# Optimization experiments

Measured on AMD Instinct MI355X. Metric: run time of the kernel, lower is better.

The kernel has to match this reference:

```python
import jax, jax.numpy as jnp
import numpy as np

K = 7        # kernel_size
G = 16       # group_number
STRIDE = 1
BN_EPS = 1e-5


def setup_inputs() -> dict:
    key = jax.random.key(0)
    ks = jax.random.split(key, 3)
    B, C, H, W = 2, 256, 56, 56
    Cr = C // 4  # reduction_ratio = 4
    x = jax.random.normal(ks[0], (B, C, H, W), dtype=jnp.float32)
    w1 = jax.random.normal(ks[1], (Cr, C), dtype=jnp.float32) * (1.0 / np.sqrt(C))
    b1 = jnp.zeros((Cr,), dtype=jnp.float32)
    gamma = jnp.ones((Cr,), dtype=jnp.float32)
    beta = jnp.zeros((Cr,), dtype=jnp.float32)
    w2 = jax.random.normal(ks[2], (K * K * G, Cr), dtype=jnp.float32) * (1.0 / np.sqrt(Cr))
    b2 = jnp.zeros((K * K * G,), dtype=jnp.float32)
    return {"x": x, "w1": w1, "b1": b1, "gamma": gamma, "beta": beta, "w2": w2, "b2": b2}


def _kernel_gen(x, w1, b1, gamma, beta, w2, b2):
    # 1x1 conv -> BatchNorm (training-mode batch stats) -> ReLU -> 1x1 conv
    t = jnp.einsum('oc,bchw->bohw', w1, x) + b1[None, :, None, None]
    mean = t.mean(axis=(0, 2, 3), keepdims=True)
    var = t.var(axis=(0, 2, 3), keepdims=True)
    t = (t - mean) * jax.lax.rsqrt(var + BN_EPS)
    t = t * gamma[None, :, None, None] + beta[None, :, None, None]
    t = jax.nn.relu(t)
    return jnp.einsum('oc,bchw->bohw', w2, t) + b2[None, :, None, None]


def reference(x, w1, b1, gamma, beta, w2, b2):
    B, C, H, W = x.shape
    nh, nw = H // STRIDE, W // STRIDE  # stride == 1 here
    # kernel generation (stride==1 -> no avg_pool)
    k = _kernel_gen(x, w1, b1, gamma, beta, w2, b2)          # (B, K*K*G, nh, nw)
    kernel = k.reshape(B, K * K, nh, nw, G)                   # raw view, as in torch
    # F.unfold with padding=K//2, stride=1 -> layout (B, C*K*K, L), c-major then k
    p = K // 2
    xp = jnp.pad(x, ((0, 0), (0, 0), (p, p), (p, p)))
    patches = jnp.stack(
        [xp[:, :, i:i + nh, j:j + nw] for i in range(K) for j in range(K)],
        axis=2)                                               # (B, C, K*K, nh, nw)
    flat = patches.reshape(B, C * K * K, nh * nw)             # == torch F.unfold
    ip = flat.reshape(B, C // G, K * K, nh, nw, G)            # raw view, as in torch
    out = (kernel[:, None] * ip).sum(axis=2)                  # (B, C//G, nh, nw, G)
    out = out.reshape(B, C, nh, nw)                           # raw view, as in torch
    return out, kernel
```

## Files before the change

kernel.cpp:

```cpp
#include <hip/hip_runtime.h>

#define HW     3136
#define C_IN   256
#define CR     64
#define KKG    784
#define NB     2
#define NPIX   6272
#define NT25   25
#define BN_EPS 1e-5f

__device__ float g_P[4 * CR * NPIX];
__device__ float g_T[CR * NPIX];
__device__ float g_bs[2 * CR * NT25];
__device__ float g_xg[16 * NPIX * 16];

__global__ __launch_bounds__(256) void k1a_conv1(const float* __restrict__ x,
                                                 const float* __restrict__ w1) {
  int p = blockIdx.x * 256 + threadIdx.x;
  if (p >= NPIX) return;
  int o0 = blockIdx.y * 4;
  int kc = blockIdx.z;
  int b  = p / HW;
  int u  = p - b * HW;

  const float* xb = x + ((size_t)(b * C_IN + kc * 64)) * HW + u;
  const float* w  = w1 + kc * 64;

  float a0 = 0.f, a1 = 0.f, a2 = 0.f, a3 = 0.f;
#pragma unroll 8
  for (int c = 0; c < 64; ++c) {
    float xv = xb[(size_t)c * HW];
    a0 += w[(o0 + 0) * C_IN + c] * xv;
    a1 += w[(o0 + 1) * C_IN + c] * xv;
    a2 += w[(o0 + 2) * C_IN + c] * xv;
    a3 += w[(o0 + 3) * C_IN + c] * xv;
  }
  float* pp = g_P + ((size_t)kc * CR + o0) * NPIX + p;
  pp[0 * NPIX] = a0; pp[1 * NPIX] = a1; pp[2 * NPIX] = a2; pp[3 * NPIX] = a3;
}

__global__ __launch_bounds__(256) void kRT(const float* __restrict__ x,
                                           const float* __restrict__ b1) {
  int p = blockIdx.x * 256 + threadIdx.x;
  if (blockIdx.y < 64) {
    int o = blockIdx.y;
    bool valid = (p < NPIX);
    float v = 0.0f;
    if (valid) {
      v = b1[o]
        + g_P[((size_t)0 * CR + o) * NPIX + p]
        + g_P[((size_t)1 * CR + o) * NPIX + p]
        + g_P[((size_t)2 * CR + o) * NPIX + p]
        + g_P[((size_t)3 * CR + o) * NPIX + p];
      g_T[(size_t)o * NPIX + p] = v;
    }
    float s  = valid ? v : 0.0f;
    float s2 = valid ? v * v : 0.0f;
#pragma unroll
    for (int off = 32; off > 0; off >>= 1) {
      s  += __shfl_down(s, off);
      s2 += __shfl_down(s2, off);
    }
    __shared__ float sd[8];
    int lane = threadIdx.x & 63, wid = threadIdx.x >> 6;
    if (lane == 0) { sd[wid] = s; sd[4 + wid] = s2; }
    __syncthreads();
    if (threadIdx.x == 0) {
      g_bs[o * NT25 + blockIdx.x]             = sd[0] + sd[1] + sd[2] + sd[3];
      g_bs[CR * NT25 + o * NT25 + blockIdx.x] = sd[4] + sd[5] + sd[6] + sd[7];
    }
  } else {
    int d = blockIdx.y - 64;
    if (p >= NPIX) return;
    int b  = (p >= HW) ? 1 : 0;
    int hw = p - b * HW;
    const float* xp = x + ((size_t)(b * C_IN + d)) * HW + hw;
    float r[16];
#pragma unroll
    for (int cg = 0; cg < 16; ++cg)
      r[cg] = xp[(size_t)cg * (16 * HW)];
    float4* dst = (float4*)(g_xg + (((size_t)d * NPIX + p) << 4));
    dst[0] = make_float4(r[0], r[1], r[2], r[3]);
    dst[1] = make_float4(r[4], r[5], r[6], r[7]);
    dst[2] = make_float4(r[8], r[9], r[10], r[11]);
    dst[3] = make_float4(r[12], r[13], r[14], r[15]);
  }
}

__global__ __launch_bounds__(256) void k3_conv2(const float* __restrict__ gamma,
                                                const float* __restrict__ beta,
                                                const float* __restrict__ w2,
                                                const float* __restrict__ b2,
                                                float* __restrict__ kout) {
  __shared__ float ssc[CR], ssh[CR];
  if (threadIdx.x < CR) {
    int o = threadIdx.x;
    float S = 0.f, S2 = 0.f;
#pragma unroll
    for (int px = 0; px < NT25; ++px) {
      S  += g_bs[o * NT25 + px];
      S2 += g_bs[CR * NT25 + o * NT25 + px];
    }
    const float invN = 1.0f / (float)NPIX;
    float mean = S * invN;
    float var  = S2 * invN - mean * mean;
    float inv  = rsqrtf(var + BN_EPS);
    float sc   = gamma[o] * inv;
    ssc[o] = sc;
    ssh[o] = beta[o] - mean * sc;
  }
  __syncthreads();

  int l  = blockIdx.x * 256 + threadIdx.x;
  if (l >= HW) return;
  int o0 = blockIdx.y * 16;
  int b  = blockIdx.z;

  float acc[16];
#pragma unroll
  for (int i = 0; i < 16; ++i) acc[i] = b2[o0 + i];

  const float* Tb = g_T + (size_t)b * HW + l;
  const float* w  = w2 + (size_t)o0 * CR;
#pragma unroll 4
  for (int c = 0; c < CR; ++c) {
    float tv = Tb[(size_t)c * NPIX];
    tv = fmaxf(tv * ssc[c] + ssh[c], 0.0f);
#pragma unroll
    for (int i = 0; i < 16; ++i)
      acc[i] += w[i * CR + c] * tv;
  }
  float* kb = kout + (size_t)(b * KKG + o0) * HW + l;
#pragma unroll
  for (int i = 0; i < 16; ++i) kb[(size_t)i * HW] = acc[i];
}

__global__ __launch_bounds__(256) void k4_invol(const float* __restrict__ kout,
                                                float* __restrict__ out) {
  int u = blockIdx.x * 256 + threadIdx.x;
  if (u >= HW) return;
  int s   = blockIdx.y;
  int bz  = blockIdx.z;
  int b   = bz >> 1;
  int cg0 = (bz & 1) * 8;

  int yrow = u / 56;
  int col  = u - yrow * 56;

  const float* kb = kout + (size_t)b * (KKG * HW) + (size_t)s * HW + u;
  const float* xg = g_xg + cg0;
  const size_t bHW16 = (size_t)(b * HW) << 4;

  float acc[8];
#pragma unroll
  for (int i = 0; i < 8; ++i) acc[i] = 0.0f;

#pragma unroll 7
  for (int kk = 0; kk < 49; ++kk) {
    int t16 = 16 * kk + s;
    int d   = t16 / 49;
    int kkp = t16 - d * 49;
    int ki  = kkp / 7;
    int kj  = kkp - ki * 7;
    int yy = yrow + ki - 3, xx = col + kj - 3;
    float kv = kb[(size_t)kk * (16 * HW)];
    int off;
    if ((unsigned)yy < 56u && (unsigned)xx < 56u) {
      off = yy * 56 + xx;
    } else {
      off = 0;
      kv = 0.0f;
    }
    const float* xp = xg + (((size_t)d * NPIX + off) << 4) + bHW16;
    float4 xa  = *(const float4*)xp;
    float4 xb4 = *(const float4*)(xp + 4);
    acc[0] += kv * xa.x;  acc[1] += kv * xa.y;
    acc[2] += kv * xa.z;  acc[3] += kv * xa.w;
    acc[4] += kv * xb4.x; acc[5] += kv * xb4.y;
    acc[6] += kv * xb4.z; acc[7] += kv * xb4.w;
  }

  float* ob = out + (size_t)b * (C_IN * HW) + ((size_t)(16 * cg0 + s)) * HW + u;
#pragma unroll
  for (int cg = 0; cg < 8; ++cg) ob[(size_t)cg * (16 * HW)] = acc[cg];
}

extern "C" void kernel_launch(void* const* d_in, const int* in_sizes, int n_in,
                              void* d_out, int out_size, void* d_ws, size_t ws_size,
                              hipStream_t stream) {
  const float* x     = (const float*)d_in[0];
  const float* w1    = (const float*)d_in[1];
  const float* b1    = (const float*)d_in[2];
  const float* gamma = (const float*)d_in[3];
  const float* beta  = (const float*)d_in[4];
  const float* w2    = (const float*)d_in[5];
  const float* b2    = (const float*)d_in[6];

  float* out  = (float*)d_out;
  float* kout = out + (size_t)NB * C_IN * HW;

  k1a_conv1<<<dim3(25, 16, 4), 256, 0, stream>>>(x, w1);
  kRT<<<dim3(25, 80), 256, 0, stream>>>(x, b1);
  k3_conv2<<<dim3(13, 49, NB), 256, 0, stream>>>(gamma, beta, w2, b2, kout);
  k4_invol<<<dim3(13, 16, 4), 256, 0, stream>>>(kout, out);
}
```

Measured before the change: 139.1 us.

## Fuse conv1 split-K and reduction into one kernel with transposed weights

Drops the split-K partial buffer: one kernel now computes the full 256-channel conv1 for 8 outputs per thread, writes T, and emits the per-tile BN partial sums. A new pre-kernel transposes w1 and w2 so the weight reads inside the conv loops are contiguous uniform loads. This removes the partial-sum round trip through global memory, at the cost of an extra launch and far fewer conv1 blocks (25x8), which lowers parallelism and makes each thread run a longer serial loop.

```diff
diff --git a/kernel.cpp b/kernel.cpp
--- a/kernel.cpp
+++ b/kernel.cpp
@@ -9,68 +9,76 @@
 #define NT25   25
 #define BN_EPS 1e-5f
 
-__device__ float g_P[4 * CR * NPIX];
 __device__ float g_T[CR * NPIX];
 __device__ float g_bs[2 * CR * NT25];
 __device__ float g_xg[16 * NPIX * 16];
-
-__global__ __launch_bounds__(256) void k1a_conv1(const float* __restrict__ x,
-                                                 const float* __restrict__ w1) {
-  int p = blockIdx.x * 256 + threadIdx.x;
-  if (p >= NPIX) return;
-  int o0 = blockIdx.y * 4;
-  int kc = blockIdx.z;
-  int b  = p / HW;
-  int u  = p - b * HW;
-
-  const float* xb = x + ((size_t)(b * C_IN + kc * 64)) * HW + u;
-  const float* w  = w1 + kc * 64;
-
-  float a0 = 0.f, a1 = 0.f, a2 = 0.f, a3 = 0.f;
+__device__ float g_w1t[C_IN * CR];
+__device__ float g_w2t[CR * KKG];
+
+__global__ __launch_bounds__(256) void k0_wt(const float* __restrict__ w1,
+                                             const float* __restrict__ w2) {
+  int idx = blockIdx.x * 256 + threadIdx.x;
+  for (int i = idx; i < 16384 + 50176; i += 25 * 256) {
+    if (i < 16384) {
+      int c = i >> 6, o = i & 63;
+      g_w1t[i] = w1[o * C_IN + c];
+    } else {
+      int j = i - 16384;
+      int c = j / KKG, o = j - c * KKG;
+      g_w2t[j] = w2[o * CR + c];
+    }
+  }
+}
+
+__global__ __launch_bounds__(256) void kA(const float* __restrict__ x,
+                                          const float* __restrict__ b1) {
+  int xt = blockIdx.x;
+  int p  = xt * 256 + threadIdx.x;
+  int y  = blockIdx.y;
+  if (y < 8) {
+    int o0 = y * 8;
+    bool valid = (p < NPIX);
+    int b = (p >= HW) ? 1 : 0;
+    int u = p - b * HW;
+    const float* xb = x + (size_t)b * (C_IN * HW) + u;
+    const float* wt = g_w1t + o0;
+
+    float acc[8];
+#pragma unroll
+    for (int i = 0; i < 8; ++i) acc[i] = b1[o0 + i];
+    if (valid) {
 #pragma unroll 8
-  for (int c = 0; c < 64; ++c) {
-    float xv = xb[(size_t)c * HW];
-    a0 += w[(o0 + 0) * C_IN + c] * xv;
-    a1 += w[(o0 + 1) * C_IN + c] * xv;
-    a2 += w[(o0 + 2) * C_IN + c] * xv;
-    a3 += w[(o0 + 3) * C_IN + c] * xv;
-  }
-  float* pp = g_P + ((size_t)kc * CR + o0) * NPIX + p;
-  pp[0 * NPIX] = a0; pp[1 * NPIX] = a1; pp[2 * NPIX] = a2; pp[3 * NPIX] = a3;
-}
-
-__global__ __launch_bounds__(256) void kRT(const float* __restrict__ x,
-                                           const float* __restrict__ b1) {
-  int p = blockIdx.x * 256 + threadIdx.x;
-  if (blockIdx.y < 64) {
-    int o = blockIdx.y;
-    bool valid = (p < NPIX);
-    float v = 0.0f;
-    if (valid) {
-      v = b1[o]
-        + g_P[((size_t)0 * CR + o) * NPIX + p]
-        + g_P[((size_t)1 * CR + o) * NPIX + p]
-        + g_P[((size_t)2 * CR + o) * NPIX + p]
-        + g_P[((size_t)3 * CR + o) * NPIX + p];
-      g_T[(size_t)o * NPIX + p] = v;
-    }
-    float s  = valid ? v : 0.0f;
-    float s2 = valid ? v * v : 0.0f;
-#pragma unroll
-    for (int off = 32; off > 0; off >>= 1) {
-      s  += __shfl_down(s, off);
-      s2 += __shfl_down(s2, off);
-    }
-    __shared__ float sd[8];
+      for (int c = 0; c < C_IN; ++c) {
+        float xv = xb[(size_t)c * HW];
+#pragma unroll
+        for (int i = 0; i < 8; ++i)
+          acc[i] += wt[c * CR + i] * xv;
+      }
+    }
+    __shared__ float sdA[8][4], sdB[8][4];
     int lane = threadIdx.x & 63, wid = threadIdx.x >> 6;
-    if (lane == 0) { sd[wid] = s; sd[4 + wid] = s2; }
+#pragma unroll
+    for (int i = 0; i < 8; ++i) {
+      float v = valid ? acc[i] : 0.0f;
+      if (valid) g_T[(size_t)(o0 + i) * NPIX + p] = v;
+      float a = v, q = v * v;
+#pragma unroll
+      for (int off = 32; off > 0; off >>= 1) {
+        a += __shfl_down(a, off);
+        q += __shfl_down(q, off);
+      }
+      if (lane == 0) { sdA[i][wid] = a; sdB[i][wid] = q; }
+    }
     __syncthreads();
-    if (threadIdx.x == 0) {
-      g_bs[o * NT25 + blockIdx.x]             = sd[0] + sd[1] + sd[2] + sd[3];
-      g_bs[CR * NT25 + o * NT25 + blockIdx.x] = sd[4] + sd[5] + sd[6] + sd[7];
+    if (threadIdx.x < 8) {
+      int i = threadIdx.x;
+      float S  = sdA[i][0] + sdA[i][1] + sdA[i][2] + sdA[i][3];
+      float S2 = sdB[i][0] + sdB[i][1] + sdB[i][2] + sdB[i][3];
+      g_bs[(o0 + i) * NT25 + xt]             = S;
+      g_bs[CR * NT25 + (o0 + i) * NT25 + xt] = S2;
     }
   } else {
-    int d = blockIdx.y - 64;
+    int d = y - 8;
     if (p >= NPIX) return;
     int b  = (p >= HW) ? 1 : 0;
     int hw = p - b * HW;
@@ -87,9 +95,8 @@
   }
 }
 
-__global__ __launch_bounds__(256) void k3_conv2(const float* __restrict__ gamma,
+__global__ __launch_bounds__(256) void kB_conv2(const float* __restrict__ gamma,
                                                 const float* __restrict__ beta,
-                                                const float* __restrict__ w2,
                                                 const float* __restrict__ b2,
                                                 float* __restrict__ kout) {
   __shared__ float ssc[CR], ssh[CR];
@@ -121,14 +128,14 @@
   for (int i = 0; i < 16; ++i) acc[i] = b2[o0 + i];
 
   const float* Tb = g_T + (size_t)b * HW + l;
-  const float* w  = w2 + (size_t)o0 * CR;
+  const float* wt = g_w2t + o0;
 #pragma unroll 4
   for (int c = 0; c < CR; ++c) {
     float tv = Tb[(size_t)c * NPIX];
     tv = fmaxf(tv * ssc[c] + ssh[c], 0.0f);
 #pragma unroll
     for (int i = 0; i < 16; ++i)
-      acc[i] += w[i * CR + c] * tv;
+      acc[i] += wt[c * KKG + i] * tv;
   }
   float* kb = kout + (size_t)(b * KKG + o0) * HW + l;
 #pragma unroll
@@ -199,8 +206,8 @@
   float* out  = (float*)d_out;
   float* kout = out + (size_t)NB * C_IN * HW;
 
-  k1a_conv1<<<dim3(25, 16, 4), 256, 0, stream>>>(x, w1);
-  kRT<<<dim3(25, 80), 256, 0, stream>>>(x, b1);
-  k3_conv2<<<dim3(13, 49, NB), 256, 0, stream>>>(gamma, beta, w2, b2, kout);
+  k0_wt<<<dim3(25), 256, 0, stream>>>(w1, w2);
+  kA<<<dim3(25, 24), 256, 0, stream>>>(x, b1);
+  kB_conv2<<<dim3(13, 49, NB), 256, 0, stream>>>(gamma, beta, b2, kout);
   k4_invol<<<dim3(13, 16, 4), 256, 0, stream>>>(kout, out);
 }
```

New measurement: 144.9 us. 4.1% more time.

## Pre-transpose conv2 weights and split involution channel groups across more blocks

Applied to the files above, without the earlier changes.

Extra blocks in the conv1 launch transpose w2 into a c-major global buffer, so conv2 reads 16 consecutive output weights per input channel instead of strided rows. The involution kernel now computes 4 channel groups per thread instead of 8 and launches twice as many blocks, which raises parallelism and lowers register pressure. In exchange, the kernel weights in kout are reloaded twice as often and there is a small extra transpose pass.

```diff
diff --git a/kernel.cpp b/kernel.cpp
--- a/kernel.cpp
+++ b/kernel.cpp
@@ -13,9 +13,19 @@
 __device__ float g_T[CR * NPIX];
 __device__ float g_bs[2 * CR * NT25];
 __device__ float g_xg[16 * NPIX * 16];
+__device__ float g_w2t[CR * KKG];
 
 __global__ __launch_bounds__(256) void k1a_conv1(const float* __restrict__ x,
-                                                 const float* __restrict__ w1) {
+                                                 const float* __restrict__ w1,
+                                                 const float* __restrict__ w2) {
+  if (blockIdx.y == 16) {
+    int idx = (blockIdx.z * 25 + blockIdx.x) * 256 + threadIdx.x;
+    for (int j = idx; j < CR * KKG; j += 100 * 256) {
+      int c = j / KKG, o = j - c * KKG;
+      g_w2t[j] = w2[o * CR + c];
+    }
+    return;
+  }
   int p = blockIdx.x * 256 + threadIdx.x;
   if (p >= NPIX) return;
   int o0 = blockIdx.y * 4;
@@ -87,9 +97,8 @@
   }
 }
 
-__global__ __launch_bounds__(256) void k3_conv2(const float* __restrict__ gamma,
+__global__ __launch_bounds__(256) void kB_conv2(const float* __restrict__ gamma,
                                                 const float* __restrict__ beta,
-                                                const float* __restrict__ w2,
                                                 const float* __restrict__ b2,
                                                 float* __restrict__ kout) {
   __shared__ float ssc[CR], ssh[CR];
@@ -121,14 +130,14 @@
   for (int i = 0; i < 16; ++i) acc[i] = b2[o0 + i];
 
   const float* Tb = g_T + (size_t)b * HW + l;
-  const float* w  = w2 + (size_t)o0 * CR;
+  const float* wt = g_w2t + o0;
 #pragma unroll 4
   for (int c = 0; c < CR; ++c) {
     float tv = Tb[(size_t)c * NPIX];
     tv = fmaxf(tv * ssc[c] + ssh[c], 0.0f);
 #pragma unroll
     for (int i = 0; i < 16; ++i)
-      acc[i] += w[i * CR + c] * tv;
+      acc[i] += wt[c * KKG + i] * tv;
   }
   float* kb = kout + (size_t)(b * KKG + o0) * HW + l;
 #pragma unroll
@@ -141,8 +150,8 @@
   if (u >= HW) return;
   int s   = blockIdx.y;
   int bz  = blockIdx.z;
-  int b   = bz >> 1;
-  int cg0 = (bz & 1) * 8;
+  int b   = bz >> 2;
+  int cg0 = (bz & 3) * 4;
 
   int yrow = u / 56;
   int col  = u - yrow * 56;
@@ -151,9 +160,7 @@
   const float* xg = g_xg + cg0;
   const size_t bHW16 = (size_t)(b * HW) << 4;
 
-  float acc[8];
-#pragma unroll
-  for (int i = 0; i < 8; ++i) acc[i] = 0.0f;
+  float acc[4] = {0.f, 0.f, 0.f, 0.f};
 
 #pragma unroll 7
   for (int kk = 0; kk < 49; ++kk) {
@@ -172,17 +179,14 @@
       kv = 0.0f;
     }
     const float* xp = xg + (((size_t)d * NPIX + off) << 4) + bHW16;
-    float4 xa  = *(const float4*)xp;
-    float4 xb4 = *(const float4*)(xp + 4);
+    float4 xa = *(const float4*)xp;
     acc[0] += kv * xa.x;  acc[1] += kv * xa.y;
     acc[2] += kv * xa.z;  acc[3] += kv * xa.w;
-    acc[4] += kv * xb4.x; acc[5] += kv * xb4.y;
-    acc[6] += kv * xb4.z; acc[7] += kv * xb4.w;
   }
 
   float* ob = out + (size_t)b * (C_IN * HW) + ((size_t)(16 * cg0 + s)) * HW + u;
 #pragma unroll
-  for (int cg = 0; cg < 8; ++cg) ob[(size_t)cg * (16 * HW)] = acc[cg];
+  for (int cg = 0; cg < 4; ++cg) ob[(size_t)cg * (16 * HW)] = acc[cg];
 }
 
 extern "C" void kernel_launch(void* const* d_in, const int* in_sizes, int n_in,
@@ -199,8 +203,8 @@
   float* out  = (float*)d_out;
   float* kout = out + (size_t)NB * C_IN * HW;
 
-  k1a_conv1<<<dim3(25, 16, 4), 256, 0, stream>>>(x, w1);
+  k1a_conv1<<<dim3(25, 17, 4), 256, 0, stream>>>(x, w1, w2);
   kRT<<<dim3(25, 80), 256, 0, stream>>>(x, b1);
-  k3_conv2<<<dim3(13, 49, NB), 256, 0, stream>>>(gamma, beta, w2, b2, kout);
-  k4_invol<<<dim3(13, 16, 4), 256, 0, stream>>>(kout, out);
-}
+  kB_conv2<<<dim3(13, 49, NB), 256, 0, stream>>>(gamma, beta, b2, kout);
+  k4_invol<<<dim3(13, 16, 8), 256, 0, stream>>>(kout, out);
+}
```

After: 149.1 us. 1.07x slower.
